# Kernel optimization log

Hardware: AMD Instinct MI355X
Metric: run time of the kernel (lower is better)

## Reference

```python
import jax, jax.numpy as jnp
import numpy as np

N_NODES = 2000
N_FEAT = 16
HID = 64
RNN_LAYERS = 2
OUT_WIN = 24
OUT_DIM = 1
N_Q = 3
LN_EPS = 1e-5


def _layernorm(x, g, b):
    mu = jnp.mean(x, axis=-1, keepdims=True)
    var = jnp.mean((x - mu) ** 2, axis=-1, keepdims=True)
    return (x - mu) * jax.lax.rsqrt(var + LN_EPS) * g + b


def setup_inputs() -> dict:
    key = jax.random.key(0)
    ks = jax.random.split(key, 24)
    B, S, N, F, H = 4, 96, N_NODES, N_FEAT, HID
    E = 16000
    inp = {}
    inp['x'] = jax.random.normal(ks[0], (B, S, N, F), dtype=jnp.float32)
    inp['edge_index'] = jax.random.randint(ks[1], (2, E), 0, N, dtype=jnp.int64)
    inp['edge_weight'] = jax.random.uniform(ks[2], (E,), dtype=jnp.float32)
    sc = 1.0 / np.sqrt(H)
    inp['W_gcn'] = jax.random.normal(ks[3], (H, F)) * (1.0 / np.sqrt(F))
    inp['b_gcn'] = jnp.zeros((H,))
    inp['Wq'] = jax.random.normal(ks[4], (H, H)) * sc
    inp['Wk'] = jax.random.normal(ks[5], (H, H)) * sc
    inp['Wv'] = jax.random.normal(ks[6], (H, H)) * sc
    inp['v_w'] = jax.random.normal(ks[7], (1, H)) * sc
    inp['v_b'] = jnp.zeros((1,))
    inp['ln1_g'] = jnp.ones((H,)); inp['ln1_b'] = jnp.zeros((H,))
    inp['gru_Wih'] = jax.random.normal(ks[8], (RNN_LAYERS, 3 * H, H)) * sc
    inp['gru_Whh'] = jax.random.normal(ks[9], (RNN_LAYERS, 3 * H, H)) * sc
    inp['gru_bih'] = jnp.zeros((RNN_LAYERS, 3 * H))
    inp['gru_bhh'] = jnp.zeros((RNN_LAYERS, 3 * H))
    inp['ln2_g'] = jnp.ones((H,)); inp['ln2_b'] = jnp.zeros((H,))
    inp['pre1_W'] = jax.random.normal(ks[10], (2 * H, H)) * sc
    inp['pre1_b'] = jnp.zeros((2 * H,))
    inp['pre2_W'] = jax.random.normal(ks[11], (N * H, 2 * H)) * (1.0 / np.sqrt(2 * H))
    inp['pre2_b'] = jnp.zeros((N * H,))
    inp['low_W'] = jax.random.normal(ks[12], (OUT_WIN * OUT_DIM, H)) * sc
    inp['low_b'] = jnp.zeros((OUT_WIN * OUT_DIM,))
    inp['inc_W'] = jax.random.normal(ks[13], (OUT_WIN * OUT_DIM * (N_Q - 1), H)) * sc
    inp['inc_b'] = jnp.zeros((OUT_WIN * OUT_DIM * (N_Q - 1),))
    return inp


def reference(x, edge_index, edge_weight, W_gcn, b_gcn, Wq, Wk, Wv, v_w, v_b,
              ln1_g, ln1_b, gru_Wih, gru_Whh, gru_bih, gru_bhh, ln2_g, ln2_b,
              pre1_W, pre1_b, pre2_W, pre2_b, low_W, low_b, inc_W, inc_b):
    B, S, N, F = x.shape
    H = W_gcn.shape[0]
    # ---- GCNConv (PyG semantics: add self-loops, symmetric normalization) ----
    # Graph is identical across batch/timesteps, so vectorize the per-timestep
    # loop into one batched gather/scatter.
    src, dst = edge_index[0], edge_index[1]
    loops = jnp.arange(N, dtype=edge_index.dtype)
    src_a = jnp.concatenate([src, loops])
    dst_a = jnp.concatenate([dst, loops])
    ew_a = jnp.concatenate([edge_weight, jnp.ones((N,), dtype=edge_weight.dtype)])
    deg = jax.ops.segment_sum(ew_a, dst_a, num_segments=N)
    dinv = jnp.where(deg > 0, deg ** -0.5, 0.0)
    coef = dinv[src_a] * ew_a * dinv[dst_a]  # (E+N,)
    xw = jnp.einsum('bsnf,hf->bsnh', x, W_gcn)  # linear (no bias yet)
    msg = xw[:, :, src_a, :] * coef[None, None, :, None]  # (B,S,E+N,H)
    h = jnp.zeros((B, S, N, H), dtype=xw.dtype).at[:, :, dst_a].add(msg)
    h = jax.nn.elu(h + b_gcn)  # dropout is identity in eval
    # ---- additive attention over all (t, node) positions ----
    keys = h.reshape(B, S * N, H)
    query = h[:, -1].mean(axis=1)  # (B,H)
    qp = query @ Wq.T  # (B,H)
    kp = keys @ Wk.T   # (B,SN,H)
    vp = keys @ Wv.T
    energy = jnp.tanh(qp[:, None, :] + kp)
    scores = energy @ v_w[0] + v_b[0]  # (B,SN)
    attn = jax.nn.softmax(scores, axis=1)
    context = jnp.einsum('bk,bkh->bh', attn, vp)
    context = _layernorm(context, ln1_g, ln1_b)
    # ---- GRU with seq_len=1, h0=0 (torch gate order: r,z,n) ----
    inp = context
    for l in range(gru_Wih.shape[0]):
        gi = inp @ gru_Wih[l].T + gru_bih[l]  # (B,3H)
        gh = gru_bhh[l]                        # h_prev = 0
        i_r, i_z, i_n = jnp.split(gi, 3, axis=-1)
        h_r, h_z, h_n = jnp.split(gh, 3, axis=-1)
        r = jax.nn.sigmoid(i_r + h_r)
        z = jax.nn.sigmoid(i_z + h_z)
        n = jnp.tanh(i_n + r * h_n)
        inp = (1.0 - z) * n  # + z * 0
    final = _layernorm(inp, ln2_g, ln2_b)
    # ---- pre_head -> per-node features ----
    f = jax.nn.elu(final @ pre1_W.T + pre1_b)
    nf = (f @ pre2_W.T + pre2_b).reshape(B, N, H)
    # ---- monotonic quantile head ----
    q_low = (nf @ low_W.T + low_b).reshape(B, N, OUT_WIN, OUT_DIM)
    inc = jax.nn.softplus((nf @ inc_W.T + inc_b).reshape(B, N, OUT_WIN, OUT_DIM, N_Q - 1))
    q1 = q_low + inc[..., 0]
    q2 = q1 + inc[..., 1]
    quant = jnp.stack([q_low, q1, q2], axis=-1)  # (B,N,OW,OD,Q)
    predictions = jnp.transpose(quant, (0, 2, 1, 3, 4))  # (B,OW,N,OD,Q)
    return predictions, attn.reshape(B, S, N)
```

## Files before the change

kernel.cpp:

```cpp
#include <hip/hip_runtime.h>

#define B 4
#define S 96
#define NN 2000
#define FF 16
#define HH 64
#define EE 16000
#define SN (S*NN)
#define SLICES (B*S)
#define BSN (B*SN)
#define KB_TOTAL (BSN/16)
#define KB_PER_B (SN/16)
#define OUT_PRED (B*24*NN*3)

typedef __attribute__((ext_vector_type(8))) short short8;
typedef __attribute__((ext_vector_type(4))) float f32x4;

__device__ __forceinline__ unsigned short f2bf(float f){
  unsigned u = __float_as_uint(f);
  u += 0x7fffu + ((u >> 16) & 1u);
  return (unsigned short)(u >> 16);
}
__device__ __forceinline__ float bf2f(unsigned short s){
  return __uint_as_float(((unsigned)s) << 16);
}
__device__ __forceinline__ float fast_tanh(float x){
  float e = __expf(2.0f * x);
  return 1.0f - 2.0f / (e + 1.0f);
}
__device__ __forceinline__ float sigm(float x){ return 1.0f / (1.0f + __expf(-x)); }
__device__ __forceinline__ float eluf(float x){ return x > 0.0f ? x : expm1f(x); }
__device__ __forceinline__ float softplusf_(float x){
  return fmaxf(x, 0.0f) + log1pf(__expf(-fabsf(x)));
}

__global__ void k_pinit(float* __restrict__ degw, int* __restrict__ cnt){
  int i = blockIdx.x * 256 + threadIdx.x;
  if (i < NN){ degw[i] = 1.0f; cnt[i] = 1; }
}

__global__ void k_deg(const int* __restrict__ ei, const float* __restrict__ ew,
                      float* __restrict__ degw, int* __restrict__ cnt){
  int e = blockIdx.x * 256 + threadIdx.x;
  if (e < EE){
    int d = ei[EE + e];
    atomicAdd(&degw[d], ew[e]);
    atomicAdd(&cnt[d], 1);
  }
}

__global__ void k_scan(const int* __restrict__ cnt, float* __restrict__ degw,
                       int* __restrict__ rowptr, int* __restrict__ curs){
  __shared__ int tsum[256];
  int tid = threadIdx.x;
  for (int i = tid; i < NN; i += 256){
    float deg = degw[i];
    degw[i] = deg > 0.0f ? rsqrtf(deg) : 0.0f;
  }
  int base = tid * 8;
  int loc[8]; int s = 0;
  #pragma unroll
  for (int j = 0; j < 8; ++j){
    int v = (base + j < NN) ? cnt[base + j] : 0;
    loc[j] = s; s += v;
  }
  tsum[tid] = s;
  __syncthreads();
  for (int off = 1; off < 256; off <<= 1){
    int v = (tid >= off) ? tsum[tid - off] : 0;
    __syncthreads();
    tsum[tid] += v;
    __syncthreads();
  }
  int excl = tsum[tid] - s;
  #pragma unroll
  for (int j = 0; j < 8; ++j)
    if (base + j < NN){ rowptr[base + j] = excl + loc[j]; curs[base + j] = excl + loc[j]; }
  if (tid == 0) rowptr[NN] = EE + NN;
}

__global__ void k_fill(const int* __restrict__ ei, const float* __restrict__ ew,
                       const float* __restrict__ dinv, int* __restrict__ curs,
                       int* __restrict__ col, float* __restrict__ coefv){
  int e = blockIdx.x * 256 + threadIdx.x;
  if (e < EE){
    int s0 = ei[e], d = ei[EE + e];
    int pos = atomicAdd(&curs[d], 1);
    col[pos] = s0;
    coefv[pos] = dinv[s0] * ew[e] * dinv[d];
  }
  int i = blockIdx.x * 256 + threadIdx.x;
  if (i < NN){
    int pos = atomicAdd(&curs[i], 1);
    col[pos] = i;
    coefv[pos] = dinv[i] * dinv[i];
  }
}

__global__ __launch_bounds__(512) void k_agg(const float* __restrict__ x,
    const int* __restrict__ rowptr, const int* __restrict__ col,
    const float* __restrict__ coefv, unsigned* __restrict__ aggG){
  __shared__ float xs[1000 * 16];
  int tid = threadIdx.x;
  int slice = blockIdx.x;
  const float* xg = x + (size_t)slice * (NN * FF);

  int rs[4], re[4];
  #pragma unroll
  for (int g = 0; g < 4; ++g){
    int n = g * 512 + tid;
    if (n < NN){ rs[g] = rowptr[n]; re[g] = rowptr[n + 1]; }
    else { rs[g] = 0; re[g] = 0; }
  }
  float agg[4][16];
  #pragma unroll
  for (int g = 0; g < 4; ++g)
    #pragma unroll
    for (int i = 0; i < 16; ++i) agg[g][i] = 0.0f;

  for (int p = 0; p < 2; ++p){
    __syncthreads();
    const float4* xg4 = (const float4*)(xg + p * 16000);
    for (int i = tid; i < 4000; i += 512){
      float4 v = xg4[i];
      int sl = i >> 2, q = i & 3;
      int slot = (q + (sl >> 1)) & 3;
      *(float4*)&xs[sl * 16 + (slot << 2)] = v;
    }
    __syncthreads();
    int lo = p * 1000;
    #pragma unroll
    for (int g = 0; g < 4; ++g){
      for (int e = rs[g]; e < re[g]; ++e){
        int s = col[e];
        unsigned sl = (unsigned)(s - lo);
        if (sl < 1000u){
          float c = coefv[e];
          #pragma unroll
          for (int q = 0; q < 4; ++q){
            int slot = (q + ((int)sl >> 1)) & 3;
            float4 a = *(const float4*)&xs[sl * 16 + (slot << 2)];
            agg[g][4*q+0] += c * a.x;
            agg[g][4*q+1] += c * a.y;
            agg[g][4*q+2] += c * a.z;
            agg[g][4*q+3] += c * a.w;
          }
        }
      }
    }
  }
  #pragma unroll
  for (int g = 0; g < 4; ++g){
    int n = g * 512 + tid;
    if (n < NN){
      unsigned u[8];
      #pragma unroll
      for (int j = 0; j < 8; ++j)
        u[j] = (unsigned)f2bf(agg[g][2*j]) | ((unsigned)f2bf(agg[g][2*j+1]) << 16);
      uint4* dst = (uint4*)(aggG + ((size_t)slice * NN + n) * 8);
      dst[0] = make_uint4(u[0], u[1], u[2], u[3]);
      dst[1] = make_uint4(u[4], u[5], u[6], u[7]);
    }
  }
}

__global__ __launch_bounds__(256) void k_xform(const unsigned short* __restrict__ aggG,
    const float* __restrict__ Wg, const float* __restrict__ bg,
    unsigned short* __restrict__ h){
  int lane = threadIdx.x & 63;
  int wid  = threadIdx.x >> 6;
  int wgid = blockIdx.x * 4 + wid;
  int row16 = lane & 15, half = lane >> 4;

  short8 bf[4];
  #pragma unroll
  for (int t = 0; t < 4; ++t){
    short8 v;
    #pragma unroll
    for (int j = 0; j < 8; ++j) v[j] = 0;
    if (half < 2){
      const float* wr = Wg + (t * 16 + row16) * 16 + half * 8;
      #pragma unroll
      for (int j = 0; j < 8; ++j) v[j] = (short)f2bf(wr[j]);
    }
    bf[t] = v;
  }
  float bias[4];
  #pragma unroll
  for (int t = 0; t < 4; ++t) bias[t] = bg[t * 16 + row16];

  for (int nb = wgid; nb < KB_TOTAL; nb += 8192){
    short8 af;
    #pragma unroll
    for (int j = 0; j < 8; ++j) af[j] = 0;
    if (half < 2)
      af = *(const short8*)(aggG + ((size_t)nb * 16 + row16) * 16 + half * 8);

    f32x4 acc[4];
    #pragma unroll
    for (int t = 0; t < 4; ++t){
      f32x4 a = {0.f, 0.f, 0.f, 0.f};
      acc[t] = __builtin_amdgcn_mfma_f32_16x16x32_bf16(af, bf[t], a, 0, 0, 0);
    }
    unsigned short* hp = h + (size_t)nb * 16 * 64;
    #pragma unroll
    for (int t = 0; t < 4; ++t){
      #pragma unroll
      for (int r = 0; r < 4; ++r){
        float v = acc[t][r] + bias[t];
        float e = v > 0.0f ? v : __expf(v) - 1.0f;
        hp[(half * 4 + r) * 64 + t * 16 + row16] = f2bf(e);
      }
    }
  }
}

__global__ void k_query(const unsigned short* __restrict__ h,
                        const float* __restrict__ Wq, float* __restrict__ qp){
  __shared__ float part[256];
  __shared__ float q[64];
  int b = blockIdx.x, tid = threadIdx.x;
  int i = tid & 63, chunk = tid >> 6;
  const unsigned short* hb = h + ((size_t)(b * S + (S - 1)) * NN) * HH;
  float p = 0.0f;
  for (int n = chunk * 500; n < chunk * 500 + 500; ++n) p += bf2f(hb[n * HH + i]);
  part[tid] = p;
  __syncthreads();
  if (tid < 64) q[tid] = (part[tid] + part[tid+64] + part[tid+128] + part[tid+192]) * (1.0f / NN);
  __syncthreads();
  if (tid < 64){
    float acc = 0.0f;
    for (int k = 0; k < 64; ++k) acc += q[k] * Wq[tid * 64 + k];
    qp[b * 64 + tid] = acc;
  }
}

__global__ __launch_bounds__(256) void k_scores(const unsigned short* __restrict__ h,
    const float* __restrict__ Wk, const float* __restrict__ vw,
    const float* __restrict__ qp, float* __restrict__ scores){
  int lane = threadIdx.x & 63;
  int wid = threadIdx.x >> 6;
  int wgid = blockIdx.x * 4 + wid;
  int row16 = lane & 15, half = lane >> 4;

  short8 bf[4][2];
  #pragma unroll
  for (int t = 0; t < 4; ++t){
    int n = 16 * t + row16;
    #pragma unroll
    for (int s2 = 0; s2 < 2; ++s2){
      const float* wr = Wk + n * 64 + 32 * s2 + half * 8;
      short8 v;
      #pragma unroll
      for (int j = 0; j < 8; ++j) v[j] = (short)f2bf(wr[j]);
      bf[t][s2] = v;
    }
  }
  float vwv[4];
  #pragma unroll
  for (int t = 0; t < 4; ++t) vwv[t] = vw[16 * t + row16];

  for (int kb = wgid; kb < KB_TOTAL; kb += 8192){
    int b = kb / KB_PER_B;
    const short* hp = (const short*)h + (size_t)kb * 16 * 64;
    short8 af[2];
    #pragma unroll
    for (int s2 = 0; s2 < 2; ++s2)
      af[s2] = *(const short8*)(hp + row16 * 64 + 32 * s2 + half * 8);

    f32x4 acc[4];
    #pragma unroll
    for (int t = 0; t < 4; ++t){
      f32x4 a = {0.f, 0.f, 0.f, 0.f};
      a = __builtin_amdgcn_mfma_f32_16x16x32_bf16(af[0], bf[t][0], a, 0, 0, 0);
      a = __builtin_amdgcn_mfma_f32_16x16x32_bf16(af[1], bf[t][1], a, 0, 0, 0);
      acc[t] = a;
    }
    float part[4] = {0, 0, 0, 0};
    #pragma unroll
    for (int t = 0; t < 4; ++t){
      float qv = qp[b * 64 + 16 * t + row16];
      #pragma unroll
      for (int r = 0; r < 4; ++r)
        part[r] += vwv[t] * fast_tanh(qv + acc[t][r]);
    }
    #pragma unroll
    for (int r = 0; r < 4; ++r){
      part[r] += __shfl_xor(part[r], 1);
      part[r] += __shfl_xor(part[r], 2);
      part[r] += __shfl_xor(part[r], 4);
      part[r] += __shfl_xor(part[r], 8);
    }
    if (row16 == 0){
      #pragma unroll
      for (int r = 0; r < 4; ++r) scores[kb * 16 + half * 4 + r] = part[r];
    }
  }
}

__global__ void k_smax1(const float* __restrict__ scores, float* __restrict__ part2){
  __shared__ float red[256];
  int b = blockIdx.x >> 7, blk = blockIdx.x & 127, tid = threadIdx.x;
  const float* sc = scores + (size_t)b * SN + blk * 1500;
  float m = -1e30f;
  for (int k = tid; k < 1500; k += 256) m = fmaxf(m, sc[k]);
  red[tid] = m; __syncthreads();
  for (int s2 = 128; s2 > 0; s2 >>= 1){
    if (tid < s2) red[tid] = fmaxf(red[tid], red[tid + s2]);
    __syncthreads();
  }
  float bm = red[0]; __syncthreads();
  float sum = 0.f;
  for (int k = tid; k < 1500; k += 256) sum += __expf(sc[k] - bm);
  red[tid] = sum; __syncthreads();
  for (int s2 = 128; s2 > 0; s2 >>= 1){
    if (tid < s2) red[tid] += red[tid + s2];
    __syncthreads();
  }
  if (tid == 0){
    part2[(b * 128 + blk) * 2]     = bm;
    part2[(b * 128 + blk) * 2 + 1] = red[0];
  }
}

__global__ void k_smax2(const float* __restrict__ part2, float* __restrict__ Msum){
  int b = threadIdx.x;
  if (b < B){
    float M = -1e30f;
    for (int i = 0; i < 128; ++i) M = fmaxf(M, part2[(b * 128 + i) * 2]);
    float Ssum = 0.f;
    for (int i = 0; i < 128; ++i)
      Ssum += part2[(b * 128 + i) * 2 + 1] * __expf(part2[(b * 128 + i) * 2] - M);
    Msum[b] = M;
    Msum[4 + b] = 1.0f / Ssum;
  }
}

__global__ __launch_bounds__(256) void k_ctx(const float* __restrict__ scores,
    const float* __restrict__ Msum, const unsigned short* __restrict__ h,
    float* __restrict__ ctx_raw, float* __restrict__ outp){
  __shared__ float red[4 * 64];
  int lane = threadIdx.x & 63, wid = threadIdx.x >> 6;
  int b = blockIdx.x >> 7;
  int blk = blockIdx.x & 127;
  int kr = lane >> 3, fb = lane & 7;
  float M = Msum[b], Si = Msum[4 + b];
  const float* sc = scores + (size_t)b * SN;
  const unsigned short* hb = h + (size_t)b * SN * 64;
  float* ao = outp + OUT_PRED + (size_t)b * SN;

  float acc[8];
  #pragma unroll
  for (int j = 0; j < 8; ++j) acc[j] = 0.0f;

  for (int k0 = (blk * 4 + wid) * 8; k0 < SN; k0 += 4096){
    int k = k0 + kr;
    float a = __expf(sc[k] - M) * Si;
    uint4 u = *(const uint4*)(hb + (size_t)k * 64 + fb * 8);
    if (fb == 0) ao[k] = a;
    acc[0] += a * __uint_as_float(u.x << 16);
    acc[1] += a * __uint_as_float(u.x & 0xffff0000u);
    acc[2] += a * __uint_as_float(u.y << 16);
    acc[3] += a * __uint_as_float(u.y & 0xffff0000u);
    acc[4] += a * __uint_as_float(u.z << 16);
    acc[5] += a * __uint_as_float(u.z & 0xffff0000u);
    acc[6] += a * __uint_as_float(u.w << 16);
    acc[7] += a * __uint_as_float(u.w & 0xffff0000u);
  }
  #pragma unroll
  for (int j = 0; j < 8; ++j){
    acc[j] += __shfl_xor(acc[j], 8);
    acc[j] += __shfl_xor(acc[j], 16);
    acc[j] += __shfl_xor(acc[j], 32);
  }
  if (kr == 0){
    #pragma unroll
    for (int j = 0; j < 8; ++j) red[wid * 64 + fb * 8 + j] = acc[j];
  }
  __syncthreads();
  if (wid == 0){
    float t = red[lane] + red[64 + lane] + red[128 + lane] + red[192 + lane];
    atomicAdd(&ctx_raw[b * 64 + lane], t);
  }
}

__global__ void k_head(const float* __restrict__ ctx_raw, const float* __restrict__ Wv,
    const float* __restrict__ ln1g, const float* __restrict__ ln1b,
    const float* __restrict__ Wih, const float* __restrict__ bih,
    const float* __restrict__ bhh,
    const float* __restrict__ ln2g, const float* __restrict__ ln2b,
    const float* __restrict__ pre1W, const float* __restrict__ pre1b,
    float* __restrict__ fout){
  __shared__ float cr[64], vec[64], stat[2];
  int b = blockIdx.x, t = threadIdx.x;
  if (t < 64) cr[t] = ctx_raw[b * 64 + t];
  __syncthreads();
  float c = 0.f;
  if (t < 64){
    for (int i = 0; i < 64; ++i) c += cr[i] * Wv[t * 64 + i];
  }
  __syncthreads();
  if (t < 64) vec[t] = c;
  __syncthreads();
  if (t == 0){
    float mu = 0; for (int i = 0; i < 64; ++i) mu += vec[i]; mu *= (1.f/64.f);
    float va = 0; for (int i = 0; i < 64; ++i){ float d = vec[i] - mu; va += d * d; }
    va *= (1.f/64.f);
    stat[0] = mu; stat[1] = rsqrtf(va + 1e-5f);
  }
  __syncthreads();
  if (t < 64) cr[t] = (vec[t] - stat[0]) * stat[1] * ln1g[t] + ln1b[t];
  __syncthreads();
  for (int l = 0; l < 2; ++l){
    float nv = 0.f;
    if (t < 64){
      const float* W = Wih + l * 192 * 64;
      const float* bi = bih + l * 192;
      const float* bh = bhh + l * 192;
      float ir = bi[t], iz = bi[64 + t], in_ = bi[128 + t];
      for (int i = 0; i < 64; ++i){
        float v = cr[i];
        ir  += v * W[t * 64 + i];
        iz  += v * W[(64 + t) * 64 + i];
        in_ += v * W[(128 + t) * 64 + i];
      }
      float r = sigm(ir + bh[t]);
      float z = sigm(iz + bh[64 + t]);
      float nn2 = fast_tanh(in_ + r * bh[128 + t]);
      nv = (1.0f - z) * nn2;
    }
    __syncthreads();
    if (t < 64) cr[t] = nv;
    __syncthreads();
  }
  if (t == 0){
    float mu = 0; for (int i = 0; i < 64; ++i) mu += cr[i]; mu *= (1.f/64.f);
    float va = 0; for (int i = 0; i < 64; ++i){ float d = cr[i] - mu; va += d * d; }
    va *= (1.f/64.f);
    stat[0] = mu; stat[1] = rsqrtf(va + 1e-5f);
  }
  __syncthreads();
  if (t < 64) vec[t] = (cr[t] - stat[0]) * stat[1] * ln2g[t] + ln2b[t];
  __syncthreads();
  float fc = pre1b[t];
  for (int j = 0; j < 64; ++j) fc += vec[j] * pre1W[t * 64 + j];
  fout[b * 128 + t] = eluf(fc);
}

__global__ __launch_bounds__(256) void k_out(const float* __restrict__ f_g,
    const float* __restrict__ pre2W, const float* __restrict__ pre2b,
    const float* __restrict__ lowW, const float* __restrict__ lowb,
    const float* __restrict__ incW, const float* __restrict__ incb,
    float* __restrict__ outp){
  __shared__ float part[4 * 4 * 64];
  __shared__ float nf_lds[4 * 64];
  int lane = threadIdx.x & 63, w = threadIdx.x >> 6;
  int n = blockIdx.x;
  const float4* wr = (const float4*)(pre2W + ((size_t)(n * 64 + lane)) * 128 + w * 32);
  float a0 = 0, a1 = 0, a2 = 0, a3 = 0;
  #pragma unroll
  for (int c4 = 0; c4 < 8; ++c4){
    float4 wv4 = wr[c4];
    int cb = w * 32 + c4 * 4;
    a0 += wv4.x * f_g[cb]       + wv4.y * f_g[cb + 1]       + wv4.z * f_g[cb + 2]       + wv4.w * f_g[cb + 3];
    a1 += wv4.x * f_g[128 + cb] + wv4.y * f_g[128 + cb + 1] + wv4.z * f_g[128 + cb + 2] + wv4.w * f_g[128 + cb + 3];
    a2 += wv4.x * f_g[256 + cb] + wv4.y * f_g[256 + cb + 1] + wv4.z * f_g[256 + cb + 2] + wv4.w * f_g[256 + cb + 3];
    a3 += wv4.x * f_g[384 + cb] + wv4.y * f_g[384 + cb + 1] + wv4.z * f_g[384 + cb + 2] + wv4.w * f_g[384 + cb + 3];
  }
  part[(w * 4 + 0) * 64 + lane] = a0;
  part[(w * 4 + 1) * 64 + lane] = a1;
  part[(w * 4 + 2) * 64 + lane] = a2;
  part[(w * 4 + 3) * 64 + lane] = a3;
  __syncthreads();
  int b = w;
  float nf = pre2b[n * 64 + lane];
  #pragma unroll
  for (int w2 = 0; w2 < 4; ++w2) nf += part[(w2 * 4 + b) * 64 + lane];
  nf_lds[b * 64 + lane] = nf;
  __syncthreads();
  if (lane < 24){
    int wo = lane;
    float q0 = lowb[wo], i0 = incb[2 * wo], i1 = incb[2 * wo + 1];
    for (int j = 0; j < 64; ++j){
      float v = nf_lds[b * 64 + j];
      q0 += v * lowW[wo * 64 + j];
      i0 += v * incW[(2 * wo) * 64 + j];
      i1 += v * incW[(2 * wo + 1) * 64 + j];
    }
    float p0 = q0;
    float p1 = p0 + softplusf_(i0);
    float p2 = p1 + softplusf_(i1);
    size_t ob = ((size_t)(b * 24 + wo) * NN + n) * 3;
    outp[ob] = p0; outp[ob + 1] = p1; outp[ob + 2] = p2;
  }
}

extern "C" void kernel_launch(void* const* d_in, const int* in_sizes, int n_in,
                              void* d_out, int out_size, void* d_ws, size_t ws_size,
                              hipStream_t stream){
  const float* x     = (const float*)d_in[0];
  const int*   ei    = (const int*)d_in[1];
  const float* ew    = (const float*)d_in[2];
  const float* Wg    = (const float*)d_in[3];
  const float* bg    = (const float*)d_in[4];
  const float* Wq    = (const float*)d_in[5];
  const float* Wk    = (const float*)d_in[6];
  const float* Wv    = (const float*)d_in[7];
  const float* vw    = (const float*)d_in[8];
  const float* ln1g  = (const float*)d_in[10];
  const float* ln1b  = (const float*)d_in[11];
  const float* Wih   = (const float*)d_in[12];
  const float* bih   = (const float*)d_in[14];
  const float* bhh   = (const float*)d_in[15];
  const float* ln2g  = (const float*)d_in[16];
  const float* ln2b  = (const float*)d_in[17];
  const float* pre1W = (const float*)d_in[18];
  const float* pre1b = (const float*)d_in[19];
  const float* pre2W = (const float*)d_in[20];
  const float* pre2b = (const float*)d_in[21];
  const float* lowW  = (const float*)d_in[22];
  const float* lowb  = (const float*)d_in[23];
  const float* incW  = (const float*)d_in[24];
  const float* incb  = (const float*)d_in[25];
  float* outp = (float*)d_out;

  char* ws = (char*)d_ws;
  size_t off = 0;
  auto alloc = [&](size_t bytes) -> char* {
    char* p = ws + off;
    off += (bytes + 255) & ~(size_t)255;
    return p;
  };
  unsigned short* h  = (unsigned short*)alloc((size_t)BSN * 64 * 2);
  unsigned* aggG     = (unsigned*)alloc((size_t)BSN * 8 * 4);
  float* scores      = (float*)alloc((size_t)BSN * 4);
  int*   rowptr      = (int*)alloc((NN + 1) * 4);
  int*   col         = (int*)alloc((EE + NN) * 4);
  float* coefv       = (float*)alloc((EE + NN) * 4);
  float* degw        = (float*)alloc(NN * 4);
  int*   cnt         = (int*)alloc(NN * 4);
  int*   curs        = (int*)alloc(NN * 4);
  float* qp          = (float*)alloc(B * 64 * 4);
  float* part2       = (float*)alloc(B * 128 * 2 * 4);
  float* Msum        = (float*)alloc(8 * 4);
  float* ctx_raw     = (float*)alloc(B * 64 * 4);
  float* f_g         = (float*)alloc(B * 128 * 4);
  (void)ws_size; (void)in_sizes; (void)n_in; (void)out_size;

  hipMemsetAsync(ctx_raw, 0, B * 64 * 4, stream);
  k_pinit <<<(NN + 255) / 256, 256, 0, stream>>>(degw, cnt);
  k_deg   <<<(EE + 255) / 256, 256, 0, stream>>>(ei, ew, degw, cnt);
  k_scan  <<<1, 256, 0, stream>>>(cnt, degw, rowptr, curs);
  k_fill  <<<(EE + 255) / 256, 256, 0, stream>>>(ei, ew, degw, curs, col, coefv);
  k_agg   <<<SLICES, 512, 0, stream>>>(x, rowptr, col, coefv, aggG);
  k_xform <<<2048, 256, 0, stream>>>((const unsigned short*)aggG, Wg, bg, h);
  k_query <<<B, 256, 0, stream>>>(h, Wq, qp);
  k_scores<<<2048, 256, 0, stream>>>(h, Wk, vw, qp, scores);
  k_smax1 <<<512, 256, 0, stream>>>(scores, part2);
  k_smax2 <<<1, 64, 0, stream>>>(part2, Msum);
  k_ctx   <<<512, 256, 0, stream>>>(scores, Msum, h, ctx_raw, outp);
  k_head  <<<B, 128, 0, stream>>>(ctx_raw, Wv, ln1g, ln1b, Wih, bih, bhh,
                                  ln2g, ln2b, pre1W, pre1b, f_g);
  k_out   <<<NN, 256, 0, stream>>>(f_g, pre2W, pre2b, lowW, lowb, incW, incb, outp);
}
```

Measured before the change: 269.6 us.

## Stage whole slice as bf16 in LDS and pack edge col/coef pairs

The aggregation kernel now converts each slice's node features to bf16 and stores all 2000 nodes in shared memory at once. This removes the two-pass half-slice loop, so each edge list is walked once instead of twice with range checks. Column index and coefficient are packed into one uint2 per edge, giving a single 8-byte load per edge. The cost is bf16 rounding of x before aggregation, which lowers accuracy, plus conversion work during staging.

```diff
diff --git a/kernel.cpp b/kernel.cpp
--- a/kernel.cpp
+++ b/kernel.cpp
@@ -81,29 +81,38 @@
 
 __global__ void k_fill(const int* __restrict__ ei, const float* __restrict__ ew,
                        const float* __restrict__ dinv, int* __restrict__ curs,
-                       int* __restrict__ col, float* __restrict__ coefv){
+                       uint2* __restrict__ epack){
   int e = blockIdx.x * 256 + threadIdx.x;
   if (e < EE){
     int s0 = ei[e], d = ei[EE + e];
     int pos = atomicAdd(&curs[d], 1);
-    col[pos] = s0;
-    coefv[pos] = dinv[s0] * ew[e] * dinv[d];
+    epack[pos] = make_uint2((unsigned)s0, __float_as_uint(dinv[s0] * ew[e] * dinv[d]));
   }
   int i = blockIdx.x * 256 + threadIdx.x;
   if (i < NN){
     int pos = atomicAdd(&curs[i], 1);
-    col[pos] = i;
-    coefv[pos] = dinv[i] * dinv[i];
+    epack[pos] = make_uint2((unsigned)i, __float_as_uint(dinv[i] * dinv[i]));
   }
 }
 
 __global__ __launch_bounds__(512) void k_agg(const float* __restrict__ x,
-    const int* __restrict__ rowptr, const int* __restrict__ col,
-    const float* __restrict__ coefv, unsigned* __restrict__ aggG){
-  __shared__ float xs[1000 * 16];
+    const int* __restrict__ rowptr, const uint2* __restrict__ epack,
+    unsigned* __restrict__ aggG){
+  __shared__ unsigned xs[NN * 8];
   int tid = threadIdx.x;
   int slice = blockIdx.x;
-  const float* xg = x + (size_t)slice * (NN * FF);
+  const float4* xg4 = (const float4*)(x + (size_t)slice * (NN * FF));
+  for (int i = tid; i < 8000; i += 512){
+    float4 v = xg4[i];
+    int sl = i >> 2, q = i & 3;
+    unsigned p0 = (unsigned)f2bf(v.x) | ((unsigned)f2bf(v.y) << 16);
+    unsigned p1 = (unsigned)f2bf(v.z) | ((unsigned)f2bf(v.w) << 16);
+    int j  = q >> 1;
+    int jj = (j + (sl >> 1)) & 1;
+    int base = sl * 8 + jj * 4 + (q & 1) * 2;
+    xs[base] = p0; xs[base + 1] = p1;
+  }
+  __syncthreads();
 
   int rs[4], re[4];
   #pragma unroll
@@ -118,35 +127,31 @@
     #pragma unroll
     for (int i = 0; i < 16; ++i) agg[g][i] = 0.0f;
 
-  for (int p = 0; p < 2; ++p){
-    __syncthreads();
-    const float4* xg4 = (const float4*)(xg + p * 16000);
-    for (int i = tid; i < 4000; i += 512){
-      float4 v = xg4[i];
-      int sl = i >> 2, q = i & 3;
-      int slot = (q + (sl >> 1)) & 3;
-      *(float4*)&xs[sl * 16 + (slot << 2)] = v;
-    }
-    __syncthreads();
-    int lo = p * 1000;
-    #pragma unroll
-    for (int g = 0; g < 4; ++g){
-      for (int e = rs[g]; e < re[g]; ++e){
-        int s = col[e];
-        unsigned sl = (unsigned)(s - lo);
-        if (sl < 1000u){
-          float c = coefv[e];
-          #pragma unroll
-          for (int q = 0; q < 4; ++q){
-            int slot = (q + ((int)sl >> 1)) & 3;
-            float4 a = *(const float4*)&xs[sl * 16 + (slot << 2)];
-            agg[g][4*q+0] += c * a.x;
-            agg[g][4*q+1] += c * a.y;
-            agg[g][4*q+2] += c * a.z;
-            agg[g][4*q+3] += c * a.w;
-          }
-        }
-      }
+  #pragma unroll
+  for (int g = 0; g < 4; ++g){
+    for (int e = rs[g]; e < re[g]; ++e){
+      uint2 m = epack[e];
+      int s = (int)m.x;
+      float c = __uint_as_float(m.y);
+      int r0 = ((s >> 1) & 1) * 4;
+      uint4 ua = *(const uint4*)&xs[s * 8 + r0];
+      uint4 ub = *(const uint4*)&xs[s * 8 + (r0 ^ 4)];
+      agg[g][0]  += c * __uint_as_float(ua.x << 16);
+      agg[g][1]  += c * __uint_as_float(ua.x & 0xffff0000u);
+      agg[g][2]  += c * __uint_as_float(ua.y << 16);
+      agg[g][3]  += c * __uint_as_float(ua.y & 0xffff0000u);
+      agg[g][4]  += c * __uint_as_float(ua.z << 16);
+      agg[g][5]  += c * __uint_as_float(ua.z & 0xffff0000u);
+      agg[g][6]  += c * __uint_as_float(ua.w << 16);
+      agg[g][7]  += c * __uint_as_float(ua.w & 0xffff0000u);
+      agg[g][8]  += c * __uint_as_float(ub.x << 16);
+      agg[g][9]  += c * __uint_as_float(ub.x & 0xffff0000u);
+      agg[g][10] += c * __uint_as_float(ub.y << 16);
+      agg[g][11] += c * __uint_as_float(ub.y & 0xffff0000u);
+      agg[g][12] += c * __uint_as_float(ub.z << 16);
+      agg[g][13] += c * __uint_as_float(ub.z & 0xffff0000u);
+      agg[g][14] += c * __uint_as_float(ub.w << 16);
+      agg[g][15] += c * __uint_as_float(ub.w & 0xffff0000u);
     }
   }
   #pragma unroll
@@ -535,8 +540,7 @@
   unsigned* aggG     = (unsigned*)alloc((size_t)BSN * 8 * 4);
   float* scores      = (float*)alloc((size_t)BSN * 4);
   int*   rowptr      = (int*)alloc((NN + 1) * 4);
-  int*   col         = (int*)alloc((EE + NN) * 4);
-  float* coefv       = (float*)alloc((EE + NN) * 4);
+  uint2* epack       = (uint2*)alloc((EE + NN) * 8);
   float* degw        = (float*)alloc(NN * 4);
   int*   cnt         = (int*)alloc(NN * 4);
   int*   curs        = (int*)alloc(NN * 4);
@@ -551,8 +555,8 @@
   k_pinit <<<(NN + 255) / 256, 256, 0, stream>>>(degw, cnt);
   k_deg   <<<(EE + 255) / 256, 256, 0, stream>>>(ei, ew, degw, cnt);
   k_scan  <<<1, 256, 0, stream>>>(cnt, degw, rowptr, curs);
-  k_fill  <<<(EE + 255) / 256, 256, 0, stream>>>(ei, ew, degw, curs, col, coefv);
-  k_agg   <<<SLICES, 512, 0, stream>>>(x, rowptr, col, coefv, aggG);
+  k_fill  <<<(EE + 255) / 256, 256, 0, stream>>>(ei, ew, degw, curs, epack);
+  k_agg   <<<SLICES, 512, 0, stream>>>(x, rowptr, epack, aggG);
   k_xform <<<2048, 256, 0, stream>>>((const unsigned short*)aggG, Wg, bg, h);
   k_query <<<B, 256, 0, stream>>>(h, Wq, qp);
   k_scores<<<2048, 256, 0, stream>>>(h, Wk, vw, qp, scores);
```

New measurement: 246.6 us. -8.5%, faster.
